# Optimization experiments

Measured on AMD Instinct MI355X. Metric: run time of the kernel, lower is better.

Reference implementation:

```python
import math
import jax, jax.numpy as jnp
import numpy as np

B, T, J, EMBED, W = 16, 243, 17, 256, 3  # D = EMBED + 1 = 257, KW = 2*W+1 = 7


def log_map0_spatial(x):
    """Lorentz log map at origin (curvature 1), returning the spatial part.
    x: [..., d+1] points on the hyperboloid. Equals log_map0(x)[..., 1:]."""
    x_t = x[..., :1]
    x_s = x[..., 1:]
    xn = jnp.clip(jnp.linalg.norm(x_s, axis=-1, keepdims=True), 1e-7, None)
    return jnp.arccosh(jnp.maximum(x_t, 1.0 + 1e-7)) / xn * x_s


def exp_map0(v):
    """Lorentz exp map at origin. v: [..., d+1] tangent vector (time comp 0)."""
    v_s = v[..., 1:]
    n = jnp.clip(jnp.linalg.norm(v_s, axis=-1, keepdims=True), 1e-7, None)
    return jnp.concatenate([jnp.cosh(n), jnp.sinh(n) / n * v_s], axis=-1)


def setup_inputs() -> dict:
    key = jax.random.key(0)
    ks = jax.random.split(key, 8)
    # valid hyperboloid points: time = sqrt(1 + ||spatial||^2)
    s = jax.random.normal(ks[0], (B, T, J, EMBED), jnp.float32) * 0.5
    t = jnp.sqrt(1.0 + jnp.sum(s * s, axis=-1, keepdims=True))
    x_seq = jnp.concatenate([t, s], axis=-1)  # [B,T,J,D]
    vel_seq = jax.random.normal(ks[1], (B, T, J, EMBED + 1), jnp.float32) * 0.1
    sc = 1.0 / math.sqrt(EMBED)
    Wq = jax.random.normal(ks[2], (EMBED, EMBED), jnp.float32) * sc
    Wk = jax.random.normal(ks[3], (EMBED, EMBED), jnp.float32) * sc
    Wv = jax.random.normal(ks[4], (EMBED, EMBED), jnp.float32) * sc
    bq = jax.random.normal(ks[5], (EMBED,), jnp.float32) * sc
    bk = jax.random.normal(ks[6], (EMBED,), jnp.float32) * sc
    bv = jax.random.normal(ks[7], (EMBED,), jnp.float32) * sc
    tau = jnp.ones((1,), jnp.float32)
    return {"x_seq": x_seq, "vel_seq": vel_seq, "tau": tau,
            "Wq": Wq, "bq": bq, "Wk": Wk, "bk": bk, "Wv": Wv, "bv": bv}


def reference(x_seq, vel_seq, tau, Wq, bq, Wk, bk, Wv, bv):
    Bb, Tt, Jj, D = x_seq.shape
    d = D - 1
    KW = 2 * W + 1
    # [B,T,J,D] -> [B*J, T, D]
    x_flat = jnp.transpose(x_seq, (0, 2, 1, 3)).reshape(Bb * Jj, Tt, D)
    spatial = log_map0_spatial(x_flat)  # [BJ, T, d]
    q = spatial @ Wq.T + bq
    k = spatial @ Wk.T + bk
    v = spatial @ Wv.T + bv
    # replicate-pad along time, build +/-W windows (fixed small loop over KW=7)
    k_pad = jnp.pad(k, ((0, 0), (W, W), (0, 0)), mode='edge')
    v_pad = jnp.pad(v, ((0, 0), (W, W), (0, 0)), mode='edge')
    k_win = jnp.stack([k_pad[:, i:i + Tt] for i in range(KW)], axis=2)  # [BJ,T,KW,d]
    v_win = jnp.stack([v_pad[:, i:i + Tt] for i in range(KW)], axis=2)
    tau_c = jnp.maximum(tau, 0.001)  # shape [1], broadcasts
    logits = jnp.einsum('btd,btwd->btw', q, k_win) / (math.sqrt(d) * tau_c)
    # mask out-of-range frames at the temporal boundaries
    frame_idx = jnp.arange(Tt)[:, None] + (jnp.arange(KW) - W)[None, :]
    boundary = (frame_idx < 0) | (frame_idx >= Tt)  # [T,KW]
    logits = jnp.where(boundary[None], -jnp.inf, logits)
    attn = jax.nn.softmax(logits, axis=-1)  # [BJ,T,KW]
    agg = jnp.einsum('btw,btwd->btd', attn, v_win)  # [BJ,T,d]
    agg_full = jnp.pad(agg, ((0, 0), (0, 0), (1, 0)))  # prepend zero time comp
    z = exp_map0(agg_full)  # [BJ,T,D]
    return jnp.transpose(z.reshape(Bb, Jj, Tt, D), (0, 2, 1, 3))
```

## Files before the change

### kernel.cpp

```cpp
#include <hip/hip_runtime.h>
#include <hip/hip_bf16.h>

#define B_   16
#define T_   243
#define J_   17
#define E_   256
#define D_   257
#define BJ_  (B_ * J_)
#define M_   (BJ_ * T_)
#define MPAD_ 66176

typedef __bf16 bf16x8 __attribute__((ext_vector_type(8)));
typedef float  f32x4  __attribute__((ext_vector_type(4)));

static __device__ __forceinline__ float bf2f(unsigned short u) {
  unsigned int v = ((unsigned int)u) << 16;
  return __builtin_bit_cast(float, v);
}
static __device__ __forceinline__ unsigned short f2bf(float f) {
  __hip_bfloat16 h = __float2bfloat16(f);
  return __builtin_bit_cast(unsigned short, h);
}
static __device__ __forceinline__ float wave_sum(float v) {
  v += __shfl_xor(v, 1);
  v += __shfl_xor(v, 2);
  v += __shfl_xor(v, 4);
  v += __shfl_xor(v, 8);
  v += __shfl_xor(v, 16);
  v += __shfl_xor(v, 32);
  return v;
}
static __device__ __forceinline__ void gload_lds16(const void* g, void* l) {
  __builtin_amdgcn_global_load_lds(
      (const __attribute__((address_space(1))) void*)g,
      (__attribute__((address_space(3))) void*)l, 16, 0, 0);
}

__global__ void fuse_w_kernel(const float* __restrict__ Wq,
                              const float* __restrict__ Wk,
                              const float* __restrict__ Wv,
                              __hip_bfloat16* __restrict__ wf) {
  int idx = blockIdx.x * 256 + threadIdx.x;
  float v = (idx < 65536) ? Wq[idx]
          : (idx < 131072) ? Wk[idx - 65536]
                           : Wv[idx - 131072];
  ((unsigned short*)wf)[idx] = f2bf(v);
}

__global__ __launch_bounds__(256) void spatial_kernel(
    const float* __restrict__ x, unsigned short* __restrict__ sp) {
  int wid  = threadIdx.x >> 6;
  int lane = threadIdx.x & 63;
  int t = blockIdx.x * 4 + wid;
  if (t >= T_) return;
  int bj = blockIdx.y;
  int b = bj / J_, j = bj % J_;
  const float* row = x + ((size_t)(b * T_ + t) * J_ + j) * D_;

  float xs[4];
  float ss = 0.f;
#pragma unroll
  for (int i = 0; i < 4; ++i) {
    xs[i] = row[1 + lane * 4 + i];
    ss += xs[i] * xs[i];
  }
  ss = wave_sum(ss);
  float xn = fmaxf(sqrtf(ss), 1e-7f);
  float xt = row[0];
  float alpha = acoshf(fmaxf(xt, 1.f + 1e-7f)) / xn;

  size_t m = (size_t)bj * T_ + t;
  ushort4 o;
  o.x = f2bf(xs[0] * alpha);
  o.y = f2bf(xs[1] * alpha);
  o.z = f2bf(xs[2] * alpha);
  o.w = f2bf(xs[3] * alpha);
  *(ushort4*)(sp + m * 256 + lane * 4) = o;
}

__global__ __launch_bounds__(256) void qkv_gemm_kernel(
    const unsigned short* __restrict__ A, const unsigned short* __restrict__ Wf,
    const float* __restrict__ bq, const float* __restrict__ bk,
    const float* __restrict__ bv, unsigned short* __restrict__ C) {
  __shared__ unsigned short lA[128 * 64];
  __shared__ unsigned short lB[128 * 64];
  int tid = threadIdx.x;
  int w = tid >> 6, lane = tid & 63;
  int wr = w >> 1, wc = w & 1;
  int m0 = blockIdx.x * 128, n0 = blockIdx.y * 128;

  int rowInWave = lane >> 3;
  int srcSlot   = (lane & 7) ^ rowInWave;

  f32x4 acc[4][4] = {};

  for (int kk = 0; kk < 4; ++kk) {
#pragma unroll
    for (int i = 0; i < 4; ++i) {
      int rl = i * 32 + w * 8 + rowInWave;
      int rgA = m0 + rl;
      if (rgA > M_ - 1) rgA = M_ - 1;
      gload_lds16(A + (size_t)rgA * 256 + kk * 64 + srcSlot * 8,
                  lA + (i * 32 + w * 8) * 64);
      int rgB = n0 + rl;
      gload_lds16(Wf + (size_t)rgB * 256 + kk * 64 + srcSlot * 8,
                  lB + (i * 32 + w * 8) * 64);
    }
    __syncthreads();

    const char* baseA = (const char*)lA;
    const char* baseB = (const char*)lB;
#pragma unroll
    for (int ki = 0; ki < 2; ++ki) {
      bf16x8 af[4], bfr[4];
#pragma unroll
      for (int mi = 0; mi < 4; ++mi) {
        int r  = wr * 64 + mi * 16 + (lane & 15);
        int cb = ki * 64 + (lane >> 4) * 16;
        af[mi] = *(const bf16x8*)(baseA + r * 128 + (cb ^ ((r & 7) << 4)));
      }
#pragma unroll
      for (int ni = 0; ni < 4; ++ni) {
        int r  = wc * 64 + ni * 16 + (lane & 15);
        int cb = ki * 64 + (lane >> 4) * 16;
        bfr[ni] = *(const bf16x8*)(baseB + r * 128 + (cb ^ ((r & 7) << 4)));
      }
#pragma unroll
      for (int mi = 0; mi < 4; ++mi)
#pragma unroll
        for (int ni = 0; ni < 4; ++ni)
          acc[mi][ni] = __builtin_amdgcn_mfma_f32_16x16x32_bf16(
              af[mi], bfr[ni], acc[mi][ni], 0, 0, 0);
    }
    __syncthreads();
  }

#pragma unroll
  for (int ni = 0; ni < 4; ++ni) {
    int col = n0 + wc * 64 + ni * 16 + (lane & 15);
    float bias = (col < 256) ? bq[col] : (col < 512) ? bk[col - 256] : bv[col - 512];
#pragma unroll
    for (int mi = 0; mi < 4; ++mi) {
      int rowb = m0 + wr * 64 + mi * 16 + ((lane >> 4) * 4);
#pragma unroll
      for (int r = 0; r < 4; ++r) {
        int row = rowb + r;
        if (row < M_)
          C[(size_t)row * 768 + col] = f2bf(acc[mi][ni][r] + bias);
      }
    }
  }
}

__global__ __launch_bounds__(256) void attn_kernel(
    const unsigned short* __restrict__ qkv, const float* __restrict__ tau,
    float* __restrict__ out) {
  int wid  = threadIdx.x >> 6;
  int lane = threadIdx.x & 63;
  int t = blockIdx.x * 4 + wid;
  if (t >= T_) return;
  int bj = blockIdx.y;
  int b = bj / J_, j = bj % J_;
  size_t mrow = (size_t)bj * T_ + t;

  float tauc = fmaxf(tau[0], 1e-3f);
  float sc = 1.f / (16.f * tauc);

  float q[4];
  {
    ushort4 qa = *(const ushort4*)(qkv + mrow * 768 + lane * 4);
    q[0] = bf2f(qa.x); q[1] = bf2f(qa.y); q[2] = bf2f(qa.z); q[3] = bf2f(qa.w);
  }

  float logit[7];
#pragma unroll
  for (int ww = 0; ww < 7; ++ww) {
    int t2 = t + ww - 3;
    float d = -INFINITY;
    if (t2 >= 0 && t2 < T_) {
      size_t m2 = (size_t)bj * T_ + t2;
      ushort4 ka = *(const ushort4*)(qkv + m2 * 768 + 256 + lane * 4);
      float p = q[0] * bf2f(ka.x) + q[1] * bf2f(ka.y) +
                q[2] * bf2f(ka.z) + q[3] * bf2f(ka.w);
      d = wave_sum(p) * sc;
    }
    logit[ww] = d;
  }

  float mx = logit[0];
#pragma unroll
  for (int ww = 1; ww < 7; ++ww) mx = fmaxf(mx, logit[ww]);
  float e[7], s = 0.f;
#pragma unroll
  for (int ww = 0; ww < 7; ++ww) {
    e[ww] = expf(logit[ww] - mx);
    s += e[ww];
  }
  float inv = 1.f / s;

  float agg[4] = {0.f, 0.f, 0.f, 0.f};
#pragma unroll
  for (int ww = 0; ww < 7; ++ww) {
    int t2 = t + ww - 3;
    if (t2 >= 0 && t2 < T_) {
      size_t m2 = (size_t)bj * T_ + t2;
      ushort4 va = *(const ushort4*)(qkv + m2 * 768 + 512 + lane * 4);
      agg[0] += e[ww] * bf2f(va.x);
      agg[1] += e[ww] * bf2f(va.y);
      agg[2] += e[ww] * bf2f(va.z);
      agg[3] += e[ww] * bf2f(va.w);
    }
  }
#pragma unroll
  for (int i = 0; i < 4; ++i) agg[i] *= inv;

  float nn = agg[0]*agg[0] + agg[1]*agg[1] + agg[2]*agg[2] + agg[3]*agg[3];
  nn = wave_sum(nn);
  float n = fmaxf(sqrtf(nn), 1e-7f);
  float scale = sinhf(n) / n;

  float* orow = out + ((size_t)(b * T_ + t) * J_ + j) * D_;
  if (lane == 0) orow[0] = coshf(n);
#pragma unroll
  for (int i = 0; i < 4; ++i) orow[1 + lane * 4 + i] = agg[i] * scale;
}

extern "C" void kernel_launch(void* const* d_in, const int* in_sizes, int n_in,
                              void* d_out, int out_size, void* d_ws, size_t ws_size,
                              hipStream_t stream) {
  const float* x   = (const float*)d_in[0];
  const float* tau = (const float*)d_in[2];
  const float* Wq  = (const float*)d_in[3];
  const float* bq  = (const float*)d_in[4];
  const float* Wk  = (const float*)d_in[5];
  const float* bk  = (const float*)d_in[6];
  const float* Wv  = (const float*)d_in[7];
  const float* bv  = (const float*)d_in[8];
  float* out = (float*)d_out;

  char* ws = (char*)d_ws;
  __hip_bfloat16* wf  = (__hip_bfloat16*)(ws);
  unsigned short* sp  = (unsigned short*)(ws + 393216);
  unsigned short* qkv = (unsigned short*)(ws + 393216 + (size_t)MPAD_ * 256 * 2);

  fuse_w_kernel<<<dim3(768), dim3(256), 0, stream>>>(Wq, Wk, Wv, wf);
  spatial_kernel<<<dim3(61, BJ_), dim3(256), 0, stream>>>(x, sp);
  qkv_gemm_kernel<<<dim3(517, 6), dim3(256), 0, stream>>>(
      sp, (const unsigned short*)wf, bq, bk, bv, qkv);
  attn_kernel<<<dim3(61, BJ_), dim3(256), 0, stream>>>(qkv, tau, out);
}
```

Baseline: 354.9 us.

## Fuse log-map into QKV GEMM with LDS-resident A tile across all N tiles

Merges the spatial log-map kernel into the QKV GEMM. Each 512-thread block computes a 128x256 bf16 A tile directly into LDS and keeps it resident while looping over all six 128-column N tiles. W tiles are double-buffered in LDS, and the output goes through an LDS staging buffer for coalesced 16-byte stores. This removes the sp intermediate round trip through global memory and the repeated A reloads, at the cost of fewer blocks (517), heavy LDS use (96KB), and serialized N tiles within a block.

```diff
diff --git a/kernel.cpp b/kernel.cpp
--- a/kernel.cpp
+++ b/kernel.cpp
@@ -8,7 +8,6 @@
 #define D_   257
 #define BJ_  (B_ * J_)
 #define M_   (BJ_ * T_)
-#define MPAD_ 66176
 
 typedef __bf16 bf16x8 __attribute__((ext_vector_type(8)));
 typedef float  f32x4  __attribute__((ext_vector_type(4)));
@@ -47,108 +46,133 @@
   ((unsigned short*)wf)[idx] = f2bf(v);
 }
 
-__global__ __launch_bounds__(256) void spatial_kernel(
-    const float* __restrict__ x, unsigned short* __restrict__ sp) {
-  int wid  = threadIdx.x >> 6;
-  int lane = threadIdx.x & 63;
-  int t = blockIdx.x * 4 + wid;
-  if (t >= T_) return;
-  int bj = blockIdx.y;
-  int b = bj / J_, j = bj % J_;
-  const float* row = x + ((size_t)(b * T_ + t) * J_ + j) * D_;
-
-  float xs[4];
-  float ss = 0.f;
-#pragma unroll
-  for (int i = 0; i < 4; ++i) {
-    xs[i] = row[1 + lane * 4 + i];
-    ss += xs[i] * xs[i];
-  }
-  ss = wave_sum(ss);
-  float xn = fmaxf(sqrtf(ss), 1e-7f);
-  float xt = row[0];
-  float alpha = acoshf(fmaxf(xt, 1.f + 1e-7f)) / xn;
-
-  size_t m = (size_t)bj * T_ + t;
-  ushort4 o;
-  o.x = f2bf(xs[0] * alpha);
-  o.y = f2bf(xs[1] * alpha);
-  o.z = f2bf(xs[2] * alpha);
-  o.w = f2bf(xs[3] * alpha);
-  *(ushort4*)(sp + m * 256 + lane * 4) = o;
-}
-
-__global__ __launch_bounds__(256) void qkv_gemm_kernel(
-    const unsigned short* __restrict__ A, const unsigned short* __restrict__ Wf,
+__global__ __launch_bounds__(512) void qkv_fused_kernel(
+    const float* __restrict__ x, const unsigned short* __restrict__ Wf,
     const float* __restrict__ bq, const float* __restrict__ bk,
     const float* __restrict__ bv, unsigned short* __restrict__ C) {
-  __shared__ unsigned short lA[128 * 64];
-  __shared__ unsigned short lB[128 * 64];
-  int tid = threadIdx.x;
-  int w = tid >> 6, lane = tid & 63;
-  int wr = w >> 1, wc = w & 1;
-  int m0 = blockIdx.x * 128, n0 = blockIdx.y * 128;
+  __shared__ __align__(16) unsigned short lA[128 * 256];
+  __shared__ __align__(16) unsigned short lW[2][128 * 64];
+
+  int tid  = threadIdx.x;
+  int w    = tid >> 6;
+  int lane = tid & 63;
+  int wr   = w >> 2;
+  int wcn  = w & 3;
+  int m0   = blockIdx.x * 128;
+
+  {
+    char* bA = (char*)lA;
+    for (int rr = 0; rr < 16; ++rr) {
+      int lr = w * 16 + rr;
+      int m  = m0 + lr; if (m > M_ - 1) m = M_ - 1;
+      int bj = m / T_;  int t = m - bj * T_;
+      int b  = bj / J_; int j = bj - b * J_;
+      const float* row = x + (size_t)((b * T_ + t) * J_ + j) * D_;
+      float xs[4], ss = 0.f;
+#pragma unroll
+      for (int i = 0; i < 4; ++i) {
+        xs[i] = row[1 + lane * 4 + i];
+        ss += xs[i] * xs[i];
+      }
+      ss = wave_sum(ss);
+      float xn = fmaxf(sqrtf(ss), 1e-7f);
+      float alpha = acoshf(fmaxf(row[0], 1.f + 1e-7f)) / xn;
+      ushort4 o;
+      o.x = f2bf(xs[0] * alpha); o.y = f2bf(xs[1] * alpha);
+      o.z = f2bf(xs[2] * alpha); o.w = f2bf(xs[3] * alpha);
+      int byte = lr * 512 + ((lane * 8) ^ ((lr & 7) << 4));
+      *(ushort4*)(bA + byte) = o;
+    }
+  }
+  __syncthreads();
 
   int rowInWave = lane >> 3;
   int srcSlot   = (lane & 7) ^ rowInWave;
 
-  f32x4 acc[4][4] = {};
-
-  for (int kk = 0; kk < 4; ++kk) {
-#pragma unroll
-    for (int i = 0; i < 4; ++i) {
-      int rl = i * 32 + w * 8 + rowInWave;
-      int rgA = m0 + rl;
-      if (rgA > M_ - 1) rgA = M_ - 1;
-      gload_lds16(A + (size_t)rgA * 256 + kk * 64 + srcSlot * 8,
-                  lA + (i * 32 + w * 8) * 64);
-      int rgB = n0 + rl;
-      gload_lds16(Wf + (size_t)rgB * 256 + kk * 64 + srcSlot * 8,
-                  lB + (i * 32 + w * 8) * 64);
+  const char* bA = (const char*)lA;
+
+  for (int nt = 0; nt < 6; ++nt) {
+    int n0 = nt * 128;
+
+    float bias[2];
+#pragma unroll
+    for (int ni = 0; ni < 2; ++ni) {
+      int colg = n0 + wcn * 32 + ni * 16 + (lane & 15);
+      bias[ni] = (colg < 256) ? bq[colg]
+               : (colg < 512) ? bk[colg - 256] : bv[colg - 512];
+    }
+
+    f32x4 acc[4][2] = {};
+
+#pragma unroll
+    for (int i = 0; i < 2; ++i) {
+      int rbase = (w * 2 + i) * 8;
+      gload_lds16(Wf + (size_t)(n0 + rbase + rowInWave) * 256 + srcSlot * 8,
+                  lW[0] + rbase * 64);
     }
     __syncthreads();
 
-    const char* baseA = (const char*)lA;
-    const char* baseB = (const char*)lB;
-#pragma unroll
-    for (int ki = 0; ki < 2; ++ki) {
-      bf16x8 af[4], bfr[4];
-#pragma unroll
-      for (int mi = 0; mi < 4; ++mi) {
-        int r  = wr * 64 + mi * 16 + (lane & 15);
-        int cb = ki * 64 + (lane >> 4) * 16;
-        af[mi] = *(const bf16x8*)(baseA + r * 128 + (cb ^ ((r & 7) << 4)));
-      }
-#pragma unroll
-      for (int ni = 0; ni < 4; ++ni) {
-        int r  = wc * 64 + ni * 16 + (lane & 15);
-        int cb = ki * 64 + (lane >> 4) * 16;
-        bfr[ni] = *(const bf16x8*)(baseB + r * 128 + (cb ^ ((r & 7) << 4)));
-      }
-#pragma unroll
-      for (int mi = 0; mi < 4; ++mi)
-#pragma unroll
-        for (int ni = 0; ni < 4; ++ni)
-          acc[mi][ni] = __builtin_amdgcn_mfma_f32_16x16x32_bf16(
-              af[mi], bfr[ni], acc[mi][ni], 0, 0, 0);
-    }
+    for (int kk = 0; kk < 4; ++kk) {
+      if (kk < 3) {
+#pragma unroll
+        for (int i = 0; i < 2; ++i) {
+          int rbase = (w * 2 + i) * 8;
+          gload_lds16(Wf + (size_t)(n0 + rbase + rowInWave) * 256 +
+                          (kk + 1) * 64 + srcSlot * 8,
+                      lW[(kk + 1) & 1] + rbase * 64);
+        }
+      }
+      const char* bW = (const char*)lW[kk & 1];
+#pragma unroll
+      for (int ki = 0; ki < 2; ++ki) {
+        bf16x8 a[4], bfr[2];
+        int cbA = kk * 128 + ki * 64 + (lane >> 4) * 16;
+#pragma unroll
+        for (int mi = 0; mi < 4; ++mi) {
+          int r = wr * 64 + mi * 16 + (lane & 15);
+          a[mi] = *(const bf16x8*)(bA + r * 512 + (cbA ^ ((r & 7) << 4)));
+        }
+        int cbB = ki * 64 + (lane >> 4) * 16;
+#pragma unroll
+        for (int ni = 0; ni < 2; ++ni) {
+          int r = wcn * 32 + ni * 16 + (lane & 15);
+          bfr[ni] = *(const bf16x8*)(bW + r * 128 + (cbB ^ ((r & 7) << 4)));
+        }
+#pragma unroll
+        for (int mi = 0; mi < 4; ++mi)
+#pragma unroll
+          for (int ni = 0; ni < 2; ++ni)
+            acc[mi][ni] = __builtin_amdgcn_mfma_f32_16x16x32_bf16(
+                a[mi], bfr[ni], acc[mi][ni], 0, 0, 0);
+      }
+      __syncthreads();
+    }
+
+    char* bC = (char*)lW[0];
+#pragma unroll
+    for (int mi = 0; mi < 4; ++mi)
+#pragma unroll
+      for (int ni = 0; ni < 2; ++ni) {
+        int col = wcn * 32 + ni * 16 + (lane & 15);
+#pragma unroll
+        for (int r = 0; r < 4; ++r) {
+          int row  = wr * 64 + mi * 16 + (lane >> 4) * 4 + r;
+          int byte = row * 256 + ((col * 2) ^ ((row & 7) << 4));
+          *(unsigned short*)(bC + byte) = f2bf(acc[mi][ni][r] + bias[ni]);
+        }
+      }
     __syncthreads();
-  }
-
-#pragma unroll
-  for (int ni = 0; ni < 4; ++ni) {
-    int col = n0 + wc * 64 + ni * 16 + (lane & 15);
-    float bias = (col < 256) ? bq[col] : (col < 512) ? bk[col - 256] : bv[col - 512];
-#pragma unroll
-    for (int mi = 0; mi < 4; ++mi) {
-      int rowb = m0 + wr * 64 + mi * 16 + ((lane >> 4) * 4);
-#pragma unroll
-      for (int r = 0; r < 4; ++r) {
-        int row = rowb + r;
-        if (row < M_)
-          C[(size_t)row * 768 + col] = f2bf(acc[mi][ni][r] + bias);
-      }
-    }
+#pragma unroll
+    for (int p = 0; p < 4; ++p) {
+      int row  = p * 32 + (tid >> 4);
+      int seg  = tid & 15;
+      int byte = row * 256 + ((seg * 16) ^ ((row & 7) << 4));
+      uint4 val = *(const uint4*)(bC + byte);
+      int gm = m0 + row;
+      if (gm < M_)
+        *(uint4*)(C + (size_t)gm * 768 + n0 + seg * 8) = val;
+    }
+    __syncthreads();
   }
 }
 
@@ -240,12 +264,10 @@
 
   char* ws = (char*)d_ws;
   __hip_bfloat16* wf  = (__hip_bfloat16*)(ws);
-  unsigned short* sp  = (unsigned short*)(ws + 393216);
-  unsigned short* qkv = (unsigned short*)(ws + 393216 + (size_t)MPAD_ * 256 * 2);
+  unsigned short* qkv = (unsigned short*)(ws + 393216);
 
   fuse_w_kernel<<<dim3(768), dim3(256), 0, stream>>>(Wq, Wk, Wv, wf);
-  spatial_kernel<<<dim3(61, BJ_), dim3(256), 0, stream>>>(x, sp);
-  qkv_gemm_kernel<<<dim3(517, 6), dim3(256), 0, stream>>>(
-      sp, (const unsigned short*)wf, bq, bk, bv, qkv);
+  qkv_fused_kernel<<<dim3(517), dim3(512), 0, stream>>>(
+      x, (const unsigned short*)wf, bq, bk, bv, qkv);
   attn_kernel<<<dim3(61, BJ_), dim3(256), 0, stream>>>(qkv, tau, out);
 }
```

Measured after the change: 343.3 us. 3.3% less time.
